# Performance work log

Measured on AMD Instinct MI355X. Metric: run time of the kernel, lower is better.

## Reference

```python
import jax, jax.numpy as jnp
import numpy as np


def setup_inputs() -> dict:
    key = jax.random.key(0)
    k1, k2, k3 = jax.random.split(key, 3)
    N, C, H, W, O = 4, 256, 64, 64, 256
    x = jax.random.normal(k1, (N, C, H, W), jnp.float32)
    # offset per forward signature: [N, H*W, 2*3*3]
    offset = jax.random.normal(k2, (N, H * W, 18), jnp.float32)
    # DeformConv weight [O, C, 3, 3], normal_init std=0.01, bias=False
    weight = jax.random.normal(k3, (O, C, 3, 3), jnp.float32) * 0.01
    return {"x": x, "offset": offset, "weight": weight}


def _deform_conv3x3(x, offset, weight):
    """Deformable conv v1: 3x3, stride 1, padding 1, dilation 1, no bias.
    x: [N,C,H,W]; offset: [N,HW,18] (permuted to [N,18,H,W] as in the module);
    weight: [O,C,3,3].
    """
    N, C, H, W = x.shape
    O = weight.shape[0]
    # module does offset.permute(0,2,1).reshape(N,-1,H,W) -> [N,18,H,W]
    off = offset.transpose(0, 2, 1).reshape(N, 9, 2, H, W)  # (dy,dx) per kernel pos
    dy, dx = off[:, :, 0], off[:, :, 1]                      # [N,9,H,W]

    # base 3x3 kernel offsets (padding=1 keeps the grid centered)
    ky = jnp.array([-1, -1, -1, 0, 0, 0, 1, 1, 1], x.dtype)
    kx = jnp.array([-1, 0, 1, -1, 0, 1, -1, 0, 1], x.dtype)
    hg = jnp.arange(H, dtype=x.dtype)[:, None]  # [H,1]
    wg = jnp.arange(W, dtype=x.dtype)[None, :]  # [1,W]
    py = hg[None, None] + ky[None, :, None, None] + dy  # [N,9,H,W] sample rows
    px = wg[None, None] + kx[None, :, None, None] + dx  # [N,9,H,W] sample cols

    y0 = jnp.floor(py)
    x0 = jnp.floor(px)
    wy = (py - y0)[:, None]  # [N,1,9,H,W]
    wx = (px - x0)[:, None]

    def gather(iy, ix):
        # zero-padded gather: out[n,c,k,h,w] = x[n,c,iy,ix] (0 if out of bounds)
        valid = (iy >= 0) & (iy < H) & (ix >= 0) & (ix < W)
        iyc = jnp.clip(iy, 0, H - 1).astype(jnp.int32)
        ixc = jnp.clip(ix, 0, W - 1).astype(jnp.int32)
        g = jax.vmap(lambda xn, yn, wn: xn[:, yn, wn])(x, iyc, ixc)  # [N,C,9,H,W]
        return g * valid[:, None].astype(x.dtype)

    v00 = gather(y0, x0)
    v01 = gather(y0, x0 + 1)
    v10 = gather(y0 + 1, x0)
    v11 = gather(y0 + 1, x0 + 1)
    # bilinear blend -> sampled columns [N,C,9,H,W]
    val = (v00 * (1 - wy) * (1 - wx) + v01 * (1 - wy) * wx
           + v10 * wy * (1 - wx) + v11 * wy * wx)
    # conv accumulate over channels and kernel positions
    return jnp.einsum('nckhw,ock->nohw', val, weight.reshape(O, C, 9))


def reference(x, offset, weight):
    return _deform_conv3x3(x, offset, weight)
```

## Files before the change

kernel.cpp:

```cpp
#include <hip/hip_runtime.h>
#include <hip/hip_fp16.h>

#define CC 256
#define OO 256
#define HH 64
#define WW 64
#define HWN 4096
#define MPB 64
#define NPB 128
#define VST 264

typedef _Float16 half8 __attribute__((ext_vector_type(8)));
typedef _Float16 half2v __attribute__((ext_vector_type(2)));
typedef float f32x4 __attribute__((ext_vector_type(4)));

__device__ __forceinline__ half2v u2h(unsigned u) {
  half2v h; __builtin_memcpy(&h, &u, 4); return h;
}
__device__ __forceinline__ unsigned h2u(half2v h) {
  unsigned u; __builtin_memcpy(&u, &h, 4); return u;
}
__device__ __forceinline__ unsigned short f2h(float f) {
  _Float16 h = (_Float16)f;
  unsigned short us; __builtin_memcpy(&us, &h, 2);
  return us;
}
__device__ __forceinline__ unsigned dupu(unsigned short us) {
  return ((unsigned)us << 16) | us;
}
__device__ __forceinline__ unsigned pk2(float a, float b) {
  half2v h = {(_Float16)a, (_Float16)b};
  return h2u(h);
}

__global__ __launch_bounds__(256) void prep_kernel(
    const float* __restrict__ x, const float* __restrict__ w,
    _Float16* __restrict__ xt, _Float16* __restrict__ wt) {
  const int bid = blockIdx.x;
  const int tid = threadIdx.x;
  if (bid < 1024) {
    __shared__ float tile[64][65];
    const int n  = bid >> 8;
    const int c0 = ((bid >> 6) & 3) * 64;
    const int s0 = (bid & 63) * 64;
    {
      int r  = tid >> 2;
      int sc = (tid & 3) * 16;
      const float* xp = x + ((size_t)(n * CC + c0 + r)) * HWN + s0 + sc;
      float4 va = *(const float4*)(xp);
      float4 vb = *(const float4*)(xp + 4);
      float4 vc = *(const float4*)(xp + 8);
      float4 vd = *(const float4*)(xp + 12);
      tile[sc + 0][r]  = va.x;  tile[sc + 1][r]  = va.y;
      tile[sc + 2][r]  = va.z;  tile[sc + 3][r]  = va.w;
      tile[sc + 4][r]  = vb.x;  tile[sc + 5][r]  = vb.y;
      tile[sc + 6][r]  = vb.z;  tile[sc + 7][r]  = vb.w;
      tile[sc + 8][r]  = vc.x;  tile[sc + 9][r]  = vc.y;
      tile[sc + 10][r] = vc.z;  tile[sc + 11][r] = vc.w;
      tile[sc + 12][r] = vd.x;  tile[sc + 13][r] = vd.y;
      tile[sc + 14][r] = vd.z;  tile[sc + 15][r] = vd.w;
    }
    __syncthreads();
    {
      int s  = tid >> 2;
      int cg = (tid & 3) * 16;
      uint4 u0, u1;
      u0.x = pk2(tile[s][cg + 0],  tile[s][cg + 1]);
      u0.y = pk2(tile[s][cg + 2],  tile[s][cg + 3]);
      u0.z = pk2(tile[s][cg + 4],  tile[s][cg + 5]);
      u0.w = pk2(tile[s][cg + 6],  tile[s][cg + 7]);
      u1.x = pk2(tile[s][cg + 8],  tile[s][cg + 9]);
      u1.y = pk2(tile[s][cg + 10], tile[s][cg + 11]);
      u1.z = pk2(tile[s][cg + 12], tile[s][cg + 13]);
      u1.w = pk2(tile[s][cg + 14], tile[s][cg + 15]);
      _Float16* op = xt + ((size_t)(n * HWN + s0 + s)) * CC + c0 + cg;
      *(uint4*)(op)     = u0;
      *(uint4*)(op + 8) = u1;
    }
  } else {
    __shared__ _Float16 wrow[9][264];
    const int o = bid - 1024;
    const float* wp = w + (size_t)o * (CC * 9);
    float v[9];
#pragma unroll
    for (int k = 0; k < 9; ++k) v[k] = wp[tid * 9 + k];
#pragma unroll
    for (int k = 0; k < 9; ++k) wrow[k][tid] = (_Float16)v[k];
    __syncthreads();
    for (int r = tid; r < 9 * 64; r += 256) {
      int k  = r >> 6;
      int c4 = (r & 63) * 4;
      *(uint2*)(wt + (size_t)k * (OO * CC) + (size_t)o * CC + c4) =
          *(const uint2*)(&wrow[k][c4]);
    }
  }
}

__global__ __launch_bounds__(256, 3) void deform_mfma_kernel(
    const _Float16* __restrict__ xt,
    const _Float16* __restrict__ wt,
    const float* __restrict__ off,
    float* __restrict__ out) {
  __shared__ __align__(16) _Float16 val_lds[MPB * VST];
  __shared__ ushort4 s_po[MPB * 9];
  __shared__ ushort4 s_pw[MPB * 9];

  const int tid  = threadIdx.x;
  const int lane = tid & 63;
  const int wv   = tid >> 6;
  const int n15  = lane & 15;
  const int quad = lane >> 4;

  const int bx    = blockIdx.x;
  const int nb    = (bx & 7) >> 1;
  const int hw0   = (bx >> 3) * MPB;
  const int obase = (bx & 1) * NPB;

  for (int e = tid; e < MPB * 9; e += 256) {
    int p = e / 9;
    int k = e - p * 9;
    int hw = hw0 + p;
    int h = hw >> 6, w = hw & 63;
    size_t ob = ((size_t)(nb * HWN + hw)) * 18 + 2 * k;
    float2 d = *(const float2*)(off + ob);
    float py = (float)(h + k / 3 - 1) + d.x;
    float px = (float)(w + k % 3 - 1) + d.y;
    float fy = floorf(py), fx = floorf(px);
    int iy = (int)fy, ix = (int)fx;
    float wy = py - fy, wx = px - fx;
    float my0 = ((unsigned)iy       < (unsigned)HH) ? 1.f : 0.f;
    float my1 = ((unsigned)(iy + 1) < (unsigned)HH) ? 1.f : 0.f;
    float mx0 = ((unsigned)ix       < (unsigned)WW) ? 1.f : 0.f;
    float mx1 = ((unsigned)(ix + 1) < (unsigned)WW) ? 1.f : 0.f;
    int iy0 = min(max(iy, 0), HH - 1), iy1 = min(max(iy + 1, 0), HH - 1);
    int ix0 = min(max(ix, 0), WW - 1), ix1 = min(max(ix + 1, 0), WW - 1);
    s_po[e] = make_ushort4((unsigned short)(iy0 * WW + ix0),
                           (unsigned short)(iy0 * WW + ix1),
                           (unsigned short)(iy1 * WW + ix0),
                           (unsigned short)(iy1 * WW + ix1));
    s_pw[e] = make_ushort4(f2h((1.f - wy) * (1.f - wx) * my0 * mx0),
                           f2h((1.f - wy) * wx         * my0 * mx1),
                           f2h(wy         * (1.f - wx) * my1 * mx0),
                           f2h(wy         * wx         * my1 * mx1));
  }

  f32x4 acc[4][2];
#pragma unroll
  for (int a = 0; a < 4; ++a)
#pragma unroll
    for (int b = 0; b < 2; ++b) acc[a][b] = (f32x4){0.f, 0.f, 0.f, 0.f};

  const _Float16* xb = xt + (size_t)nb * HWN * CC;
  const int j = lane & 31;
  const int ph = lane >> 5;

  for (int k = 0; k < 9; ++k) {
    __syncthreads();

    const _Float16* wb = wt + ((size_t)(k * OO + obase + wv * 32)) * CC;
    half8 bfr[8][2];
#pragma unroll
    for (int ks = 0; ks < 8; ++ks)
#pragma unroll
      for (int nt = 0; nt < 2; ++nt)
        bfr[ks][nt] = *(const half8*)(wb + (size_t)(nt * 16 + n15) * CC + ks * 32 + quad * 8);

#pragma unroll
    for (int i = 0; i < 8; ++i) {
      int p = i * 8 + wv * 2 + ph;
      int idx = p * 9 + k;
      ushort4 o4 = s_po[idx];
      ushort4 hw4 = s_pw[idx];
      half2v w00 = u2h(dupu(hw4.x)), w01 = u2h(dupu(hw4.y));
      half2v w10 = u2h(dupu(hw4.z)), w11 = u2h(dupu(hw4.w));
      const _Float16* cb = xb + (size_t)j * 8;
      uint4 v00 = *(const uint4*)(cb + (size_t)o4.x * CC);
      uint4 v01 = *(const uint4*)(cb + (size_t)o4.y * CC);
      uint4 v10 = *(const uint4*)(cb + (size_t)o4.z * CC);
      uint4 v11 = *(const uint4*)(cb + (size_t)o4.w * CC);
      uint4 r;
      r.x = h2u(u2h(v00.x) * w00 + u2h(v01.x) * w01 + u2h(v10.x) * w10 + u2h(v11.x) * w11);
      r.y = h2u(u2h(v00.y) * w00 + u2h(v01.y) * w01 + u2h(v10.y) * w10 + u2h(v11.y) * w11);
      r.z = h2u(u2h(v00.z) * w00 + u2h(v01.z) * w01 + u2h(v10.z) * w10 + u2h(v11.z) * w11);
      r.w = h2u(u2h(v00.w) * w00 + u2h(v01.w) * w01 + u2h(v10.w) * w10 + u2h(v11.w) * w11);
      *(uint4*)(val_lds + p * VST + j * 8) = r;
    }
    __syncthreads();

#pragma unroll
    for (int ks = 0; ks < 8; ++ks) {
      half8 afr[4];
#pragma unroll
      for (int mt = 0; mt < 4; ++mt)
        afr[mt] = *(const half8*)(val_lds + (mt * 16 + n15) * VST + ks * 32 + quad * 8);
#pragma unroll
      for (int mt = 0; mt < 4; ++mt)
#pragma unroll
        for (int nt = 0; nt < 2; ++nt)
          acc[mt][nt] = __builtin_amdgcn_mfma_f32_16x16x32_f16(
              afr[mt], bfr[ks][nt], acc[mt][nt], 0, 0, 0);
    }
  }

#pragma unroll
  for (int mt = 0; mt < 4; ++mt)
#pragma unroll
    for (int nt = 0; nt < 2; ++nt) {
      int o  = obase + wv * 32 + nt * 16 + n15;
      int px = hw0 + mt * 16 + quad * 4;
      *(f32x4*)(out + ((size_t)nb * OO + o) * HWN + px) = acc[mt][nt];
    }
}

extern "C" void kernel_launch(void* const* d_in, const int* in_sizes, int n_in,
                              void* d_out, int out_size, void* d_ws, size_t ws_size,
                              hipStream_t stream) {
  const float* x   = (const float*)d_in[0];
  const float* off = (const float*)d_in[1];
  const float* w   = (const float*)d_in[2];
  float* out = (float*)d_out;

  _Float16* wt = (_Float16*)d_ws;
  _Float16* xt = wt + 589824;

  prep_kernel<<<1024 + 256, 256, 0, stream>>>(x, w, xt, wt);
  deform_mfma_kernel<<<(4 * HWN / MPB) * (OO / NPB), 256, 0, stream>>>(xt, wt, off, out);
}
```

Baseline: 137.4 us.

## Switch to 512-thread blocks covering all outputs with 32-pixel tiles

Each block now runs 8 waves that cover all 256 output channels for a 32-pixel tile, instead of two blocks splitting the outputs over 64 pixels. This removes the duplicate bilinear sampling that both output halves used to do. The sync pattern is reordered with custom barriers so the next tap is sampled after the MFMA work, and the grid shrinks to 512 blocks. In exchange, per-block weight loads are amortised over fewer pixels, and the larger block size with the 4-blocks-per-CU launch bound may limit occupancy.

Result: slower. 152.6 us (+11.1%).

```diff
diff --git a/kernel.cpp b/kernel.cpp
--- a/kernel.cpp
+++ b/kernel.cpp
@@ -6,8 +6,7 @@
 #define HH 64
 #define WW 64
 #define HWN 4096
-#define MPB 64
-#define NPB 128
+#define MPB 32
 #define VST 264
 
 typedef _Float16 half8 __attribute__((ext_vector_type(8)));
@@ -31,6 +30,13 @@
 __device__ __forceinline__ unsigned pk2(float a, float b) {
   half2v h = {(_Float16)a, (_Float16)b};
   return h2u(h);
+}
+
+__device__ __forceinline__ void vsync() {
+  __builtin_amdgcn_sched_barrier(0);
+  asm volatile("s_waitcnt lgkmcnt(0)" ::: "memory");
+  __builtin_amdgcn_s_barrier();
+  __builtin_amdgcn_sched_barrier(0);
 }
 
 __global__ __launch_bounds__(256) void prep_kernel(
@@ -96,7 +102,7 @@
   }
 }
 
-__global__ __launch_bounds__(256, 3) void deform_mfma_kernel(
+__global__ __launch_bounds__(512, 4) void deform_mfma_kernel(
     const _Float16* __restrict__ xt,
     const _Float16* __restrict__ wt,
     const float* __restrict__ off,
@@ -111,12 +117,15 @@
   const int n15  = lane & 15;
   const int quad = lane >> 4;
 
-  const int bx    = blockIdx.x;
-  const int nb    = (bx & 7) >> 1;
-  const int hw0   = (bx >> 3) * MPB;
-  const int obase = (bx & 1) * NPB;
-
-  for (int e = tid; e < MPB * 9; e += 256) {
+  const int bx  = blockIdx.x;
+  const int xcd = bx & 7;
+  const int nb  = xcd >> 1;
+  const int hw0 = (((xcd & 1) << 6) | (bx >> 3)) * MPB;
+
+  const int o0 = wv * 32;
+
+  if (tid < MPB * 9) {
+    int e = tid;
     int p = e / 9;
     int k = e - p * 9;
     int hw = hw0 + p;
@@ -144,31 +153,21 @@
                            f2h(wy         * wx         * my1 * mx1));
   }
 
-  f32x4 acc[4][2];
-#pragma unroll
-  for (int a = 0; a < 4; ++a)
+  f32x4 acc[2][2];
+#pragma unroll
+  for (int a = 0; a < 2; ++a)
 #pragma unroll
     for (int b = 0; b < 2; ++b) acc[a][b] = (f32x4){0.f, 0.f, 0.f, 0.f};
 
   const _Float16* xb = xt + (size_t)nb * HWN * CC;
-  const int j = lane & 31;
-  const int ph = lane >> 5;
-
-  for (int k = 0; k < 9; ++k) {
-    __syncthreads();
-
-    const _Float16* wb = wt + ((size_t)(k * OO + obase + wv * 32)) * CC;
-    half8 bfr[8][2];
-#pragma unroll
-    for (int ks = 0; ks < 8; ++ks)
-#pragma unroll
-      for (int nt = 0; nt < 2; ++nt)
-        bfr[ks][nt] = *(const half8*)(wb + (size_t)(nt * 16 + n15) * CC + ks * 32 + quad * 8);
-
-#pragma unroll
-    for (int i = 0; i < 8; ++i) {
-      int p = i * 8 + wv * 2 + ph;
-      int idx = p * 9 + k;
+  const int j    = tid & 31;
+  const int slot = tid >> 5;
+
+  auto sample_tap = [&](int kk) {
+#pragma unroll
+    for (int i = 0; i < 2; ++i) {
+      int p = i * 16 + slot;
+      int idx = p * 9 + kk;
       ushort4 o4 = s_po[idx];
       ushort4 hw4 = s_pw[idx];
       half2v w00 = u2h(dupu(hw4.x)), w01 = u2h(dupu(hw4.y));
@@ -185,28 +184,46 @@
       r.w = h2u(u2h(v00.w) * w00 + u2h(v01.w) * w01 + u2h(v10.w) * w10 + u2h(v11.w) * w11);
       *(uint4*)(val_lds + p * VST + j * 8) = r;
     }
-    __syncthreads();
-
-#pragma unroll
-    for (int ks = 0; ks < 8; ++ks) {
-      half8 afr[4];
-#pragma unroll
-      for (int mt = 0; mt < 4; ++mt)
-        afr[mt] = *(const half8*)(val_lds + (mt * 16 + n15) * VST + ks * 32 + quad * 8);
-#pragma unroll
-      for (int mt = 0; mt < 4; ++mt)
+  };
+
+  __syncthreads();
+  sample_tap(0);
+  vsync();
+
+  for (int k = 0; k < 9; ++k) {
+    const _Float16* wb = wt + ((size_t)(k * OO + o0)) * CC;
+    half8 bfr[2][8];
+#pragma unroll
+    for (int nt = 0; nt < 2; ++nt)
+#pragma unroll
+      for (int ksg = 0; ksg < 8; ++ksg)
+        bfr[nt][ksg] = *(const half8*)(wb + (size_t)(nt * 16 + n15) * CC + ksg * 32 + quad * 8);
+    __builtin_amdgcn_sched_barrier(0);
+
+#pragma unroll
+    for (int ksg = 0; ksg < 8; ++ksg) {
+      half8 afr[2];
+#pragma unroll
+      for (int mt = 0; mt < 2; ++mt)
+        afr[mt] = *(const half8*)(val_lds + (mt * 16 + n15) * VST + ksg * 32 + quad * 8);
+#pragma unroll
+      for (int mt = 0; mt < 2; ++mt)
 #pragma unroll
         for (int nt = 0; nt < 2; ++nt)
           acc[mt][nt] = __builtin_amdgcn_mfma_f32_16x16x32_f16(
-              afr[mt], bfr[ks][nt], acc[mt][nt], 0, 0, 0);
-    }
+              afr[mt], bfr[nt][ksg], acc[mt][nt], 0, 0, 0);
+    }
+
+    vsync();
+    if (k < 8) sample_tap(k + 1);
+    vsync();
   }
 
 #pragma unroll
-  for (int mt = 0; mt < 4; ++mt)
+  for (int mt = 0; mt < 2; ++mt)
 #pragma unroll
     for (int nt = 0; nt < 2; ++nt) {
-      int o  = obase + wv * 32 + nt * 16 + n15;
+      int o  = o0 + nt * 16 + n15;
       int px = hw0 + mt * 16 + quad * 4;
       *(f32x4*)(out + ((size_t)nb * OO + o) * HWN + px) = acc[mt][nt];
     }
@@ -224,5 +241,5 @@
   _Float16* xt = wt + 589824;
 
   prep_kernel<<<1024 + 256, 256, 0, stream>>>(x, w, xt, wt);
-  deform_mfma_kernel<<<(4 * HWN / MPB) * (OO / NPB), 256, 0, stream>>>(xt, wt, off, out);
-}
+  deform_mfma_kernel<<<512, 512, 0, stream>>>(xt, wt, off, out);
+}
```
